# Optimization experiments

Measured on AMD Instinct MI355X. Metric: run time of the kernel, lower is better.

Reference implementation:

```python
import jax, jax.numpy as jnp
import numpy as np


def setup_inputs() -> dict:
    key = jax.random.key(0)
    k1, k2, k3, k4 = jax.random.split(key, 4)
    B, D, U = 16, 2048, 37
    inputs = jax.random.normal(k1, (B, D), dtype=jnp.float32)
    matrix = jax.random.normal(k2, (D, D), dtype=jnp.float32) * 0.05
    weight = jax.random.normal(k3, (U, D, D), dtype=jnp.float32) * 0.05
    bias = jax.random.normal(k4, (U,), dtype=jnp.float32) * 0.05
    return {"inputs": inputs, "matrix": matrix, "weight": weight, "bias": bias}


def reference(inputs, matrix, weight, bias):
    # inputs: (B, D); matrix: (D, D); weight: (U, D, D); bias: (U,)
    B, D = inputs.shape
    idx = jnp.arange(D)
    # maps = ones((B, D, D)) with per-row diagonal replaced by inputs[b]
    maps = jnp.ones((B, D, D), dtype=inputs.dtype).at[:, idx, idx].set(inputs)
    # masked multiply by learned matrix (broadcast over batch) then relu
    masked = jax.nn.relu(matrix[None, :, :] * maps)  # (B, D, D)
    # outer-product-then-reduce collapses to a direct contraction per unit:
    # conv[b, u] = sum_ij masked[b, i, j] * weight[u, i, j]
    conv = jnp.einsum('bij,uij->bu', masked, weight)
    return conv + bias[None, :]
```

## Files before the change

kernel.cpp:

```cpp
#include <hip/hip_runtime.h>

constexpr int BB = 16;
constexpr int D  = 2048;
constexpr int U  = 37;
constexpr long long DD = (long long)D * D;

constexpr int TPB = 256;
constexpr int BLOCKS_PER_U = 128;
constexpr int F4_PER_CHUNK = (int)(DD / BLOCKS_PER_U / 4);
constexpr int ITERS = F4_PER_CHUNK / TPB;

__global__ __launch_bounds__(TPB) void base_reduce_kernel(
    const float* __restrict__ matrix,
    const float* __restrict__ weight,
    float* __restrict__ base)
{
    const int chunk = blockIdx.x;
    const int u     = blockIdx.y;

    const float4* __restrict__ m4 = (const float4*)matrix;
    const float4* __restrict__ w4 = (const float4*)(weight + (long long)u * DD);

    long long idx = (long long)chunk * F4_PER_CHUNK + threadIdx.x;

    float acc = 0.f;
#pragma unroll 8
    for (int it = 0; it < ITERS; ++it) {
        float4 m = m4[idx + (long long)it * TPB];
        float4 w = w4[idx + (long long)it * TPB];
        acc = fmaf(fmaxf(m.x, 0.f), w.x, acc);
        acc = fmaf(fmaxf(m.y, 0.f), w.y, acc);
        acc = fmaf(fmaxf(m.z, 0.f), w.z, acc);
        acc = fmaf(fmaxf(m.w, 0.f), w.w, acc);
    }

#pragma unroll
    for (int off = 32; off > 0; off >>= 1)
        acc += __shfl_down(acc, off, 64);

    __shared__ float smem[TPB / 64];
    if ((threadIdx.x & 63) == 0) smem[threadIdx.x >> 6] = acc;
    __syncthreads();
    if (threadIdx.x == 0) {
        float t = 0.f;
#pragma unroll
        for (int w = 0; w < TPB / 64; ++w) t += smem[w];
        atomicAdd(&base[u], t);
    }
}

__global__ __launch_bounds__(TPB) void diag_finish_kernel(
    const float* __restrict__ inputs,
    const float* __restrict__ matrix,
    const float* __restrict__ weight,
    const float* __restrict__ bias,
    const float* __restrict__ base,
    float* __restrict__ out)
{
    const int u = blockIdx.x;
    const int b = blockIdx.y;

    float acc = 0.f;
    for (int i = threadIdx.x; i < D; i += TPB) {
        float m = matrix[(long long)i * (D + 1)];
        float w = weight[(long long)u * DD + (long long)i * (D + 1)];
        float x = inputs[b * D + i];
        acc += (fmaxf(m * x, 0.f) - fmaxf(m, 0.f)) * w;
    }

#pragma unroll
    for (int off = 32; off > 0; off >>= 1)
        acc += __shfl_down(acc, off, 64);

    __shared__ float smem[TPB / 64];
    if ((threadIdx.x & 63) == 0) smem[threadIdx.x >> 6] = acc;
    __syncthreads();
    if (threadIdx.x == 0) {
        float t = 0.f;
#pragma unroll
        for (int w = 0; w < TPB / 64; ++w) t += smem[w];
        out[b * U + u] = t + base[u] + bias[u];
    }
}

extern "C" void kernel_launch(void* const* d_in, const int* in_sizes, int n_in,
                              void* d_out, int out_size, void* d_ws, size_t ws_size,
                              hipStream_t stream) {
    const float* inputs = (const float*)d_in[0];
    const float* matrix = (const float*)d_in[1];
    const float* weight = (const float*)d_in[2];
    const float* bias   = (const float*)d_in[3];
    float* out  = (float*)d_out;
    float* base = (float*)d_ws;

    hipMemsetAsync(base, 0, U * sizeof(float), stream);

    base_reduce_kernel<<<dim3(BLOCKS_PER_U, U), TPB, 0, stream>>>(matrix, weight, base);
    diag_finish_kernel<<<dim3(U, BB), TPB, 0, stream>>>(inputs, matrix, weight, bias, base, out);
}
```

Measured before the change: 805.3 us.

## Reuse relu(matrix) tile in registers across all units, write per-block partials

Each block now loads and relus its slice of matrix once into registers, then loops over all 37 weight units, instead of re-reading matrix once per unit. Per-unit block sums go to a partials buffer that the finish kernel reduces, removing the memset and global atomics. This roughly halves the bytes read, but runs only 512 blocks with a serial unit loop, which lowers occupancy and memory-level parallelism.

```diff
diff --git a/kernel.cpp b/kernel.cpp
--- a/kernel.cpp
+++ b/kernel.cpp
@@ -6,33 +6,76 @@
 constexpr long long DD = (long long)D * D;
 
 constexpr int TPB = 256;
-constexpr int BLOCKS_PER_U = 128;
-constexpr int F4_PER_CHUNK = (int)(DD / BLOCKS_PER_U / 4);
-constexpr int ITERS = F4_PER_CHUNK / TPB;
+constexpr int C   = 512;
+constexpr int F4_PER_BLOCK  = (int)(DD / 4 / C);
+constexpr int F4_PER_THREAD = F4_PER_BLOCK / TPB;
 
 __global__ __launch_bounds__(TPB) void base_reduce_kernel(
     const float* __restrict__ matrix,
     const float* __restrict__ weight,
-    float* __restrict__ base)
+    float* __restrict__ partial)
 {
-    const int chunk = blockIdx.x;
-    const int u     = blockIdx.y;
+    const int c = blockIdx.x;
+    const long long base4 = (long long)c * F4_PER_BLOCK + threadIdx.x;
+    const float4* __restrict__ m4 = (const float4*)matrix;
 
-    const float4* __restrict__ m4 = (const float4*)matrix;
-    const float4* __restrict__ w4 = (const float4*)(weight + (long long)u * DD);
+    float4 m[F4_PER_THREAD];
+#pragma unroll
+    for (int it = 0; it < F4_PER_THREAD; ++it) {
+        float4 t = m4[base4 + (long long)it * TPB];
+        m[it].x = fmaxf(t.x, 0.f);
+        m[it].y = fmaxf(t.y, 0.f);
+        m[it].z = fmaxf(t.z, 0.f);
+        m[it].w = fmaxf(t.w, 0.f);
+    }
 
-    long long idx = (long long)chunk * F4_PER_CHUNK + threadIdx.x;
+    __shared__ float lpart[U];
+    if (threadIdx.x < U) lpart[threadIdx.x] = 0.f;
+    __syncthreads();
+
+    for (int u = 0; u < U; ++u) {
+        const float4* __restrict__ w4 = (const float4*)(weight + (long long)u * DD);
+        float acc = 0.f;
+#pragma unroll
+        for (int it = 0; it < F4_PER_THREAD; ++it) {
+            float4 w = w4[base4 + (long long)it * TPB];
+            acc = fmaf(m[it].x, w.x, acc);
+            acc = fmaf(m[it].y, w.y, acc);
+            acc = fmaf(m[it].z, w.z, acc);
+            acc = fmaf(m[it].w, w.w, acc);
+        }
+#pragma unroll
+        for (int off = 32; off > 0; off >>= 1)
+            acc += __shfl_down(acc, off, 64);
+        if ((threadIdx.x & 63) == 0)
+            atomicAdd(&lpart[u], acc);
+    }
+
+    __syncthreads();
+    if (threadIdx.x < U)
+        partial[(long long)threadIdx.x * C + c] = lpart[threadIdx.x];
+}
+
+__global__ __launch_bounds__(TPB) void diag_finish_kernel(
+    const float* __restrict__ inputs,
+    const float* __restrict__ matrix,
+    const float* __restrict__ weight,
+    const float* __restrict__ bias,
+    const float* __restrict__ partial,
+    float* __restrict__ out)
+{
+    const int u = blockIdx.x;
+    const int b = blockIdx.y;
 
     float acc = 0.f;
-#pragma unroll 8
-    for (int it = 0; it < ITERS; ++it) {
-        float4 m = m4[idx + (long long)it * TPB];
-        float4 w = w4[idx + (long long)it * TPB];
-        acc = fmaf(fmaxf(m.x, 0.f), w.x, acc);
-        acc = fmaf(fmaxf(m.y, 0.f), w.y, acc);
-        acc = fmaf(fmaxf(m.z, 0.f), w.z, acc);
-        acc = fmaf(fmaxf(m.w, 0.f), w.w, acc);
+    for (int i = threadIdx.x; i < D; i += TPB) {
+        float mm = matrix[(long long)i * (D + 1)];
+        float w  = weight[(long long)u * DD + (long long)i * (D + 1)];
+        float x  = inputs[b * D + i];
+        acc += (fmaxf(mm * x, 0.f) - fmaxf(mm, 0.f)) * w;
     }
+    for (int c = threadIdx.x; c < C; c += TPB)
+        acc += partial[(long long)u * C + c];
 
 #pragma unroll
     for (int off = 32; off > 0; off >>= 1)
@@ -45,41 +88,7 @@
         float t = 0.f;
 #pragma unroll
         for (int w = 0; w < TPB / 64; ++w) t += smem[w];
-        atomicAdd(&base[u], t);
-    }
-}
-
-__global__ __launch_bounds__(TPB) void diag_finish_kernel(
-    const float* __restrict__ inputs,
-    const float* __restrict__ matrix,
-    const float* __restrict__ weight,
-    const float* __restrict__ bias,
-    const float* __restrict__ base,
-    float* __restrict__ out)
-{
-    const int u = blockIdx.x;
-    const int b = blockIdx.y;
-
-    float acc = 0.f;
-    for (int i = threadIdx.x; i < D; i += TPB) {
-        float m = matrix[(long long)i * (D + 1)];
-        float w = weight[(long long)u * DD + (long long)i * (D + 1)];
-        float x = inputs[b * D + i];
-        acc += (fmaxf(m * x, 0.f) - fmaxf(m, 0.f)) * w;
-    }
-
-#pragma unroll
-    for (int off = 32; off > 0; off >>= 1)
-        acc += __shfl_down(acc, off, 64);
-
-    __shared__ float smem[TPB / 64];
-    if ((threadIdx.x & 63) == 0) smem[threadIdx.x >> 6] = acc;
-    __syncthreads();
-    if (threadIdx.x == 0) {
-        float t = 0.f;
-#pragma unroll
-        for (int w = 0; w < TPB / 64; ++w) t += smem[w];
-        out[b * U + u] = t + base[u] + bias[u];
+        out[b * U + u] = t + bias[u];
     }
 }
 
@@ -90,11 +99,10 @@
     const float* matrix = (const float*)d_in[1];
     const float* weight = (const float*)d_in[2];
     const float* bias   = (const float*)d_in[3];
-    float* out  = (float*)d_out;
-    float* base = (float*)d_ws;
+    float* out     = (float*)d_out;
+    float* partial = (float*)d_ws;
 
-    hipMemsetAsync(base, 0, U * sizeof(float), stream);
-
-    base_reduce_kernel<<<dim3(BLOCKS_PER_U, U), TPB, 0, stream>>>(matrix, weight, base);
-    diag_finish_kernel<<<dim3(U, BB), TPB, 0, stream>>>(inputs, matrix, weight, bias, base, out);
+    base_reduce_kernel<<<dim3(C), TPB, 0, stream>>>(matrix, weight, partial);
+    diag_finish_kernel<<<dim3(U, BB), TPB, 0, stream>>>(inputs, matrix, weight, bias,
+                                                        partial, out);
 }
```

Result: no change. 802.0 us (-0.4%).
